# Kernel optimization log

Hardware: AMD Instinct MI355X
Metric: run time of the kernel (lower is better)

Reference implementation:

```python
import jax, jax.numpy as jnp
import numpy as np

N, F, D, K, H, O = 100000, 128, 16, 8, 256, 256  # nodes, feat, degree, num_hash, hash_dim, out_dim


def setup_inputs() -> dict:
    key = jax.random.key(0)
    k1, k2, k3, k4, k5 = jax.random.split(key, 5)
    x = jax.random.normal(k1, (N, F), dtype=jnp.float32)
    nbr_idx = jax.random.randint(k2, (N, D), 0, N, dtype=jnp.int32)
    # fixed sign hash matrices, one per hasher: {+1,-1}^{F x H}
    R = (jax.random.uniform(k3, (K, F, H)) > 0.5).astype(jnp.float32) * 2.0 - 1.0
    lim = float(np.sqrt(6.0 / (K * H + O)))  # xavier_uniform for Linear(K*H, O)
    Ws = jax.random.uniform(k4, (O, K * H), jnp.float32, -lim, lim)
    Wn = jax.random.uniform(k5, (O, K * H), jnp.float32, -lim, lim)
    bias = jnp.zeros((O,), dtype=jnp.float32)
    return {"x": x, "nbr_idx": nbr_idx, "R": R, "Ws": Ws, "Wn": Wn, "bias": bias}


def reference(x, nbr_idx, R, Ws, Wn, bias):
    n, f = x.shape
    k, _, h = R.shape
    # gather neighbor feats [N, D, F] and degree-mean -> [N, F]
    # (hashing is linear, so mean(hash(neigh)) == hash(mean(neigh)))
    neigh_mean = jnp.mean(x[nbr_idx], axis=1)
    # hash with all K hashers and concatenate streams: [N, K*H]
    hashed_neigh = jnp.einsum('nf,kfh->nkh', neigh_mean, R).reshape(n, k * h)
    hashed_self = jnp.einsum('nf,kfh->nkh', x, R).reshape(n, k * h)
    out = hashed_neigh @ Wn.T + hashed_self @ Ws.T + bias
    return jax.nn.elu(out)
```

## Files before the change

kernel.cpp:

```cpp
#include <hip/hip_runtime.h>
#include <hip/hip_bf16.h>
#include <math.h>

#define NN 100000
#define FF 128
#define DD 16
#define KK 8
#define HH 256
#define OO 256
#define KH 2048

using frag_t  = __attribute__((ext_vector_type(8))) short;
using f32x4   = __attribute__((ext_vector_type(4))) float;
using ushort8 = __attribute__((ext_vector_type(8))) unsigned short;

static __device__ __forceinline__ float blo(unsigned int u) {
    union { unsigned int i; float f; } v; v.i = u << 16; return v.f;
}
static __device__ __forceinline__ float bhi(unsigned int u) {
    union { unsigned int i; float f; } v; v.i = u & 0xffff0000u; return v.f;
}
static __device__ __forceinline__ unsigned short f2bf(float f) {
    union { float f; unsigned int i; } v; v.f = f;
    unsigned int x = v.i;
    x += 0x7fffu + ((x >> 16) & 1u);
    return (unsigned short)(x >> 16);
}
static __device__ __forceinline__ unsigned int pk2(float a, float b) {
    return (unsigned int)f2bf(a) | ((unsigned int)f2bf(b) << 16);
}

__global__ __launch_bounds__(512) void k_prep(const float* __restrict__ x,
                                              const float* __restrict__ R,
                                              const float* __restrict__ Ws,
                                              const float* __restrict__ Wn,
                                              unsigned short* __restrict__ xb,
                                              unsigned short* __restrict__ Bbf) {
    __shared__ __align__(16) unsigned short Aw[64][72];
    __shared__ __align__(16) unsigned short Bw[128][72];
    int b = blockIdx.x;
    int t = threadIdx.x;
    if (b >= 8) {
        int g = (b - 8) * 512 + t;
        const float4* xv = (const float4*)x;
        float4 a = xv[2 * g], c = xv[2 * g + 1];
        ushort8 o;
        o[0] = f2bf(a.x); o[1] = f2bf(a.y); o[2] = f2bf(a.z); o[3] = f2bf(a.w);
        o[4] = f2bf(c.x); o[5] = f2bf(c.y); o[6] = f2bf(c.z); o[7] = f2bf(c.w);
        *(ushort8*)(xb + (size_t)g * 8) = o;
        return;
    }
    const int w = b >> 2, ot = b & 3;
    const float* W = (w == 0) ? Wn : Ws;
    int lane = t & 63, wv = t >> 6;
    int wo = wv >> 2, wf = wv & 3;
    int l15 = lane & 15, quad = lane >> 4;
    f32x4 acc[2][2] = {};
    for (int kt = 0; kt < 32; ++kt) {
        __syncthreads();
#pragma unroll
        for (int s = 0; s < 2; ++s) {
            int c = s * 512 + t;
            int row = c >> 4, c4 = c & 15;
            float4 v = *(const float4*)(W + (size_t)(ot * 64 + row) * KH + kt * 64 + c4 * 4);
            uint2 p; p.x = pk2(v.x, v.y); p.y = pk2(v.z, v.w);
            *(uint2*)&Aw[row][c4 * 4] = p;
        }
#pragma unroll
        for (int s = 0; s < 4; ++s) {
            int c = s * 512 + t;
            int row = c >> 4, c4 = c & 15;
            float4 v = *(const float4*)(R + (size_t)(kt >> 2) * 32768
                                          + (size_t)row * 256 + (kt & 3) * 64 + c4 * 4);
            uint2 p; p.x = pk2(v.x, v.y); p.y = pk2(v.z, v.w);
            *(uint2*)&Bw[row][c4 * 4] = p;
        }
        __syncthreads();
#pragma unroll
        for (int k2 = 0; k2 < 2; ++k2) {
            frag_t af[2], bfr[2];
#pragma unroll
            for (int i = 0; i < 2; ++i)
                af[i] = *(const frag_t*)&Aw[wo * 32 + i * 16 + l15][k2 * 32 + quad * 8];
#pragma unroll
            for (int j = 0; j < 2; ++j)
                bfr[j] = *(const frag_t*)&Bw[wf * 32 + j * 16 + l15][k2 * 32 + quad * 8];
#pragma unroll
            for (int i = 0; i < 2; ++i)
#pragma unroll
                for (int j = 0; j < 2; ++j)
                    acc[i][j] = __builtin_amdgcn_mfma_f32_16x16x32_bf16(af[i], bfr[j], acc[i][j], 0, 0, 0);
        }
    }
#pragma unroll
    for (int j = 0; j < 2; ++j) {
        int f = wf * 32 + j * 16 + l15;
#pragma unroll
        for (int i = 0; i < 2; ++i) {
            int o0 = ot * 64 + wo * 32 + i * 16 + quad * 4;
#pragma unroll
            for (int r = 0; r < 4; ++r)
                Bbf[(size_t)(o0 + r) * 256 + w * 128 + f] = f2bf(acc[i][j][r]);
        }
    }
}

__global__ __launch_bounds__(512, 4) void k_fused(const unsigned short* __restrict__ xb,
                                                  const int* __restrict__ nbr,
                                                  const unsigned short* __restrict__ Bw,
                                                  const float* __restrict__ bias,
                                                  float* __restrict__ C) {
    __shared__ __align__(16) char smraw[64 * 264 * 2];
    unsigned short (*Als)[264] = (unsigned short (*)[264])smraw;
    float* Fls = (float*)smraw;
    const int FLS_W = 260;

    int m0 = blockIdx.x * 64;
    int t = threadIdx.x;
    int lane = t & 63, wv = t >> 6;
    int l15 = lane & 15, quad = lane >> 4;
    int l16 = lane & 15, r4 = lane >> 4;
    int selbase = (lane & 48) << 2;

#pragma unroll
    for (int g = 0; g < 2; ++g) {
        int row = wv * 8 + g * 4 + r4;
        int node = m0 + row; if (node >= NN) node = NN - 1;
        int myidx = nbr[(size_t)node * 16 + l16];
        uint4 selfv = *(const uint4*)(xb + (size_t)node * 128 + l16 * 8);
        float s[8] = {0.f, 0.f, 0.f, 0.f, 0.f, 0.f, 0.f, 0.f};
#pragma unroll
        for (int h = 0; h < 2; ++h) {
            uint4 gv[8];
#pragma unroll
            for (int d = 0; d < 8; ++d) {
                int bi = __builtin_amdgcn_ds_bpermute(selbase + ((h * 8 + d) << 2), myidx);
                gv[d] = *(const uint4*)(xb + (size_t)bi * 128 + l16 * 8);
            }
#pragma unroll
            for (int d = 0; d < 8; ++d) {
                s[0] += blo(gv[d].x); s[1] += bhi(gv[d].x);
                s[2] += blo(gv[d].y); s[3] += bhi(gv[d].y);
                s[4] += blo(gv[d].z); s[5] += bhi(gv[d].z);
                s[6] += blo(gv[d].w); s[7] += bhi(gv[d].w);
            }
        }
        ushort8 o;
#pragma unroll
        for (int k = 0; k < 8; ++k) o[k] = f2bf(s[k] * 0.0625f);
        *(ushort8*)&Als[row][l16 * 8] = o;
        *(uint4*)&Als[row][128 + l16 * 8] = selfv;
    }
    __syncthreads();

    f32x4 acc[4][2] = {};
#pragma unroll 1
    for (int kt = 0; kt < 4; ++kt) {
#pragma unroll
        for (int k2 = 0; k2 < 2; ++k2) {
            frag_t bfr[2], af[4];
#pragma unroll
            for (int j = 0; j < 2; ++j)
                bfr[j] = *(const frag_t*)(Bw + (size_t)(wv * 32 + j * 16 + l15) * 256
                                             + kt * 64 + k2 * 32 + quad * 8);
#pragma unroll
            for (int i = 0; i < 4; ++i)
                af[i] = *(const frag_t*)&Als[i * 16 + l15][kt * 64 + k2 * 32 + quad * 8];
#pragma unroll
            for (int i = 0; i < 4; ++i)
#pragma unroll
                for (int j = 0; j < 2; ++j)
                    acc[i][j] = __builtin_amdgcn_mfma_f32_16x16x32_bf16(af[i], bfr[j], acc[i][j], 0, 0, 0);
        }
    }

    float bv[2];
#pragma unroll
    for (int j = 0; j < 2; ++j) bv[j] = bias[wv * 32 + j * 16 + l15];
#pragma unroll
    for (int p = 0; p < 2; ++p) {
        __syncthreads();
#pragma unroll
        for (int ii = 0; ii < 2; ++ii) {
            int i = p * 2 + ii;
#pragma unroll
            for (int j = 0; j < 2; ++j) {
                int col = wv * 32 + j * 16 + l15;
#pragma unroll
                for (int r = 0; r < 4; ++r) {
                    int lr = ii * 16 + quad * 4 + r;
                    float v = acc[i][j][r] + bv[j];
                    v = (v > 0.f) ? v : (__expf(v) - 1.0f);
                    Fls[lr * FLS_W + col] = v;
                }
            }
        }
        __syncthreads();
#pragma unroll
        for (int q = 0; q < 4; ++q) {
            int f4 = q * 512 + t;
            int lr = f4 >> 6, c4 = f4 & 63;
            int grow = m0 + p * 32 + lr;
            if (grow < NN)
                *(float4*)(C + (size_t)grow * 256 + c4 * 4) = *(const float4*)&Fls[lr * FLS_W + c4 * 4];
        }
    }
}

extern "C" void kernel_launch(void* const* d_in, const int* in_sizes, int n_in,
                              void* d_out, int out_size, void* d_ws, size_t ws_size,
                              hipStream_t stream) {
    const float* x    = (const float*)d_in[0];
    const int*   nbr  = (const int*)d_in[1];
    const float* R    = (const float*)d_in[2];
    const float* Ws   = (const float*)d_in[3];
    const float* Wn   = (const float*)d_in[4];
    const float* bias = (const float*)d_in[5];
    float* out = (float*)d_out;

    char* ws = (char*)d_ws;
    unsigned short* xb  = (unsigned short*)(ws);
    unsigned short* Bbf = (unsigned short*)(ws + 25600000);

    hipLaunchKernelGGL(k_prep,  dim3(3133), dim3(512), 0, stream, x, R, Ws, Wn, xb, Bbf);
    hipLaunchKernelGGL(k_fused, dim3(1563), dim3(512), 0, stream, xb, nbr, Bbf, bias, out);
}
```

Baseline: 269.7 us.

## Gather neighbor features in FP8, prefetch prep tiles, use nontemporal loads/stores

The prep kernel now also writes an FP8 e4m3 copy of x, and the fused kernel gathers its 16 neighbors from that copy, halving the bytes of random gather traffic. The prep GEMM prefetches the next W/R tile into registers before the current tile is consumed, and the fused kernel uses nontemporal loads for self rows and indices and nontemporal stores for the output. This trades extra prep writes and reduced precision of neighbor means (e4m3 quantization) for lower gather bandwidth.

```diff
diff --git a/kernel.cpp b/kernel.cpp
--- a/kernel.cpp
+++ b/kernel.cpp
@@ -12,14 +12,11 @@
 
 using frag_t  = __attribute__((ext_vector_type(8))) short;
 using f32x4   = __attribute__((ext_vector_type(4))) float;
+using f32x2   = __attribute__((ext_vector_type(2))) float;
 using ushort8 = __attribute__((ext_vector_type(8))) unsigned short;
-
-static __device__ __forceinline__ float blo(unsigned int u) {
-    union { unsigned int i; float f; } v; v.i = u << 16; return v.f;
-}
-static __device__ __forceinline__ float bhi(unsigned int u) {
-    union { unsigned int i; float f; } v; v.i = u & 0xffff0000u; return v.f;
-}
+using uv4     = __attribute__((ext_vector_type(4))) unsigned int;
+using uv2     = __attribute__((ext_vector_type(2))) unsigned int;
+
 static __device__ __forceinline__ unsigned short f2bf(float f) {
     union { float f; unsigned int i; } v; v.f = f;
     unsigned int x = v.i;
@@ -30,11 +27,65 @@
     return (unsigned int)f2bf(a) | ((unsigned int)f2bf(b) << 16);
 }
 
+#if defined(__has_builtin)
+#if __has_builtin(__builtin_amdgcn_cvt_pk_f32_fp8) && __has_builtin(__builtin_amdgcn_cvt_pk_fp8_f32)
+#define FP8_HW 1
+#endif
+#endif
+#ifndef FP8_HW
+#define FP8_HW 0
+#endif
+
+static __device__ __forceinline__ float e4m3f(unsigned int b) {
+    unsigned int s = (b & 0x80u) << 24;
+    unsigned int em = b & 0x7fu;
+    bool den = (b & 0x78u) == 0;
+    union { unsigned int u; float f; } v;
+    v.u = s | ((em << 20) + ((den ? 121u : 120u) << 23));
+    float f = v.f;
+    if (den) f -= (s ? -0.015625f : 0.015625f);
+    return f;
+}
+static __device__ __forceinline__ unsigned int f2e4m3(float f) {
+    union { float f; unsigned int u; } v; v.f = f;
+    unsigned int s = (v.u >> 24) & 0x80u;
+    float a = fabsf(f);
+    if (!(a < 448.f)) return s | 0x7Eu;
+    if (a < 0.015625f) {
+        int m = (int)rintf(a * 512.f);
+        return s | (unsigned int)m;
+    }
+    union { float f; unsigned int u; } w; w.f = a;
+    unsigned int u = w.u + 0x7FFFFu + ((w.u >> 20) & 1u);
+    return s | (((u >> 23) - 120u) << 3) | ((u >> 20) & 7u);
+}
+template <int SEL>
+static __device__ __forceinline__ f32x2 dec2(unsigned int w) {
+#if FP8_HW
+    return __builtin_amdgcn_cvt_pk_f32_fp8((int)w, SEL != 0);
+#else
+    f32x2 r;
+    r[0] = e4m3f((w >> (SEL * 16)) & 0xffu);
+    r[1] = e4m3f((w >> (SEL * 16 + 8)) & 0xffu);
+    return r;
+#endif
+}
+static __device__ __forceinline__ unsigned int enc4(float x0, float x1, float x2, float x3) {
+#if FP8_HW
+    int r = __builtin_amdgcn_cvt_pk_fp8_f32(x0, x1, 0, false);
+    r = __builtin_amdgcn_cvt_pk_fp8_f32(x2, x3, r, true);
+    return (unsigned int)r;
+#else
+    return f2e4m3(x0) | (f2e4m3(x1) << 8) | (f2e4m3(x2) << 16) | (f2e4m3(x3) << 24);
+#endif
+}
+
 __global__ __launch_bounds__(512) void k_prep(const float* __restrict__ x,
                                               const float* __restrict__ R,
                                               const float* __restrict__ Ws,
                                               const float* __restrict__ Wn,
                                               unsigned short* __restrict__ xb,
+                                              unsigned char* __restrict__ xb8,
                                               unsigned short* __restrict__ Bbf) {
     __shared__ __align__(16) unsigned short Aw[64][72];
     __shared__ __align__(16) unsigned short Bw[128][72];
@@ -48,6 +99,10 @@
         o[0] = f2bf(a.x); o[1] = f2bf(a.y); o[2] = f2bf(a.z); o[3] = f2bf(a.w);
         o[4] = f2bf(c.x); o[5] = f2bf(c.y); o[6] = f2bf(c.z); o[7] = f2bf(c.w);
         *(ushort8*)(xb + (size_t)g * 8) = o;
+        uv2 q;
+        q.x = enc4(a.x, a.y, a.z, a.w);
+        q.y = enc4(c.x, c.y, c.z, c.w);
+        *(uv2*)(xb8 + (size_t)g * 8) = q;
         return;
     }
     const int w = b >> 2, ot = b & 3;
@@ -55,25 +110,40 @@
     int lane = t & 63, wv = t >> 6;
     int wo = wv >> 2, wf = wv & 3;
     int l15 = lane & 15, quad = lane >> 4;
+    int rA[2], cA[2], rB[4], cB[4];
+#pragma unroll
+    for (int s = 0; s < 2; ++s) { int c0 = s * 512 + t; rA[s] = c0 >> 4; cA[s] = c0 & 15; }
+#pragma unroll
+    for (int s = 0; s < 4; ++s) { int c0 = s * 512 + t; rB[s] = c0 >> 4; cB[s] = c0 & 15; }
+    float4 av[2], bv[4];
+#pragma unroll
+    for (int s = 0; s < 2; ++s)
+        av[s] = *(const float4*)(W + (size_t)(ot * 64 + rA[s]) * KH + cA[s] * 4);
+#pragma unroll
+    for (int s = 0; s < 4; ++s)
+        bv[s] = *(const float4*)(R + (size_t)rB[s] * 256 + cB[s] * 4);
     f32x4 acc[2][2] = {};
     for (int kt = 0; kt < 32; ++kt) {
         __syncthreads();
 #pragma unroll
         for (int s = 0; s < 2; ++s) {
-            int c = s * 512 + t;
-            int row = c >> 4, c4 = c & 15;
-            float4 v = *(const float4*)(W + (size_t)(ot * 64 + row) * KH + kt * 64 + c4 * 4);
-            uint2 p; p.x = pk2(v.x, v.y); p.y = pk2(v.z, v.w);
-            *(uint2*)&Aw[row][c4 * 4] = p;
+            uint2 p; p.x = pk2(av[s].x, av[s].y); p.y = pk2(av[s].z, av[s].w);
+            *(uint2*)&Aw[rA[s]][cA[s] * 4] = p;
         }
 #pragma unroll
         for (int s = 0; s < 4; ++s) {
-            int c = s * 512 + t;
-            int row = c >> 4, c4 = c & 15;
-            float4 v = *(const float4*)(R + (size_t)(kt >> 2) * 32768
-                                          + (size_t)row * 256 + (kt & 3) * 64 + c4 * 4);
-            uint2 p; p.x = pk2(v.x, v.y); p.y = pk2(v.z, v.w);
-            *(uint2*)&Bw[row][c4 * 4] = p;
+            uint2 p; p.x = pk2(bv[s].x, bv[s].y); p.y = pk2(bv[s].z, bv[s].w);
+            *(uint2*)&Bw[rB[s]][cB[s] * 4] = p;
+        }
+        if (kt < 31) {
+            int k1 = kt + 1;
+#pragma unroll
+            for (int s = 0; s < 2; ++s)
+                av[s] = *(const float4*)(W + (size_t)(ot * 64 + rA[s]) * KH + k1 * 64 + cA[s] * 4);
+#pragma unroll
+            for (int s = 0; s < 4; ++s)
+                bv[s] = *(const float4*)(R + (size_t)(k1 >> 2) * 32768
+                                           + (size_t)rB[s] * 256 + (k1 & 3) * 64 + cB[s] * 4);
         }
         __syncthreads();
 #pragma unroll
@@ -106,6 +176,7 @@
 }
 
 __global__ __launch_bounds__(512, 4) void k_fused(const unsigned short* __restrict__ xb,
+                                                  const unsigned char* __restrict__ xb8,
                                                   const int* __restrict__ nbr,
                                                   const unsigned short* __restrict__ Bw,
                                                   const float* __restrict__ bias,
@@ -126,30 +197,32 @@
     for (int g = 0; g < 2; ++g) {
         int row = wv * 8 + g * 4 + r4;
         int node = m0 + row; if (node >= NN) node = NN - 1;
-        int myidx = nbr[(size_t)node * 16 + l16];
-        uint4 selfv = *(const uint4*)(xb + (size_t)node * 128 + l16 * 8);
+        int myidx = __builtin_nontemporal_load(nbr + (size_t)node * 16 + l16);
+        uv4 selfv = __builtin_nontemporal_load(
+            (const uv4*)(xb + (size_t)node * 128 + l16 * 8));
         float s[8] = {0.f, 0.f, 0.f, 0.f, 0.f, 0.f, 0.f, 0.f};
 #pragma unroll
         for (int h = 0; h < 2; ++h) {
-            uint4 gv[8];
+            uv2 gv[8];
 #pragma unroll
             for (int d = 0; d < 8; ++d) {
                 int bi = __builtin_amdgcn_ds_bpermute(selbase + ((h * 8 + d) << 2), myidx);
-                gv[d] = *(const uint4*)(xb + (size_t)bi * 128 + l16 * 8);
+                gv[d] = *(const uv2*)(xb8 + (size_t)bi * 128 + l16 * 8);
             }
 #pragma unroll
             for (int d = 0; d < 8; ++d) {
-                s[0] += blo(gv[d].x); s[1] += bhi(gv[d].x);
-                s[2] += blo(gv[d].y); s[3] += bhi(gv[d].y);
-                s[4] += blo(gv[d].z); s[5] += bhi(gv[d].z);
-                s[6] += blo(gv[d].w); s[7] += bhi(gv[d].w);
+                f32x2 p;
+                p = dec2<0>(gv[d].x); s[0] += p[0]; s[1] += p[1];
+                p = dec2<1>(gv[d].x); s[2] += p[0]; s[3] += p[1];
+                p = dec2<0>(gv[d].y); s[4] += p[0]; s[5] += p[1];
+                p = dec2<1>(gv[d].y); s[6] += p[0]; s[7] += p[1];
             }
         }
         ushort8 o;
 #pragma unroll
         for (int k = 0; k < 8; ++k) o[k] = f2bf(s[k] * 0.0625f);
         *(ushort8*)&Als[row][l16 * 8] = o;
-        *(uint4*)&Als[row][128 + l16 * 8] = selfv;
+        *(uv4*)&Als[row][128 + l16 * 8] = selfv;
     }
     __syncthreads();
 
@@ -202,7 +275,8 @@
             int lr = f4 >> 6, c4 = f4 & 63;
             int grow = m0 + p * 32 + lr;
             if (grow < NN)
-                *(float4*)(C + (size_t)grow * 256 + c4 * 4) = *(const float4*)&Fls[lr * FLS_W + c4 * 4];
+                __builtin_nontemporal_store(*(const f32x4*)&Fls[lr * FLS_W + c4 * 4],
+                                            (f32x4*)(C + (size_t)grow * 256 + c4 * 4));
         }
     }
 }
@@ -220,8 +294,9 @@
 
     char* ws = (char*)d_ws;
     unsigned short* xb  = (unsigned short*)(ws);
-    unsigned short* Bbf = (unsigned short*)(ws + 25600000);
-
-    hipLaunchKernelGGL(k_prep,  dim3(3133), dim3(512), 0, stream, x, R, Ws, Wn, xb, Bbf);
-    hipLaunchKernelGGL(k_fused, dim3(1563), dim3(512), 0, stream, xb, nbr, Bbf, bias, out);
-}
+    unsigned char*  xb8 = (unsigned char*)(ws + 25600000);
+    unsigned short* Bbf = (unsigned short*)(ws + 38400000);
+
+    hipLaunchKernelGGL(k_prep,  dim3(3133), dim3(512), 0, stream, x, R, Ws, Wn, xb, xb8, Bbf);
+    hipLaunchKernelGGL(k_fused, dim3(1563), dim3(512), 0, stream, xb, xb8, nbr, Bbf, bias, out);
+}
```

Measured after the change: 237.1 us. 12.1% less time.
